# Performance work log

Hardware: AMD Instinct MI355X
Metric: run time of the kernel (lower is better)

## Reference

```python
import jax, jax.numpy as jnp
import numpy as np

N = 102400      # total agents across all groups
GROUP = 50      # agents per group
G = N // GROUP  # 2048 groups
E = 128         # embedding_dim
H = 512         # h_dim


def setup_inputs() -> dict:
    key = jax.random.key(0)
    k1, k2, k3, k4, k5, k6 = jax.random.split(key, 6)
    hist_enc = jax.random.normal(k1, (N, H), dtype=jnp.float32)
    hist_pos_batch = jax.random.normal(k2, (N, 2), dtype=jnp.float32)
    # group boundaries: 0, 50, 100, ..., N  (len = G+1)
    seq_start_end = (jnp.arange(G + 1, dtype=jnp.int32) * GROUP)
    # spatial_embedding: Linear(2, E)
    Ws = jax.random.normal(k3, (2, E), dtype=jnp.float32) * (1.0 / np.sqrt(2.0))
    bs = jax.random.normal(k4, (E,), dtype=jnp.float32) * 0.01
    # mlp_pre_pool: Linear(E + H, H)
    Wm = jax.random.normal(k5, (E + H, H), dtype=jnp.float32) * (1.0 / np.sqrt(E + H))
    bm = jax.random.normal(k6, (H,), dtype=jnp.float32) * 0.01
    return {
        "hist_enc": hist_enc,
        "hist_pos_batch": hist_pos_batch,
        "seq_start_end": seq_start_end,
        "Ws": Ws, "bs": bs, "Wm": Wm, "bm": bm,
    }


def reference(hist_enc, hist_pos_batch, seq_start_end, Ws, bs, Wm, bm):
    # The original torch loop builds all n^2 pairs per group but keeps only
    # curr_pool_h[0:1], i.e. row i=0 -> pooled vector for the group's FIRST agent.
    # rel[i=0, j] = pos[j] - pos[start]; hidden index is j; max over j.
    n = hist_enc.shape[0]
    num_groups = seq_start_end.shape[0] - 1
    # segment id of each agent: group g covers [sse[g], sse[g+1])
    seg_ids = jnp.searchsorted(seq_start_end, jnp.arange(n, dtype=seq_start_end.dtype), side="right") - 1
    starts = seq_start_end[:-1]                      # [G]
    anchor = hist_pos_batch[starts][seg_ids]         # [N,2] pos of group's first agent
    rel = hist_pos_batch - anchor                    # [N,2]
    emb = jax.nn.relu(rel @ Ws + bs)                 # [N,E]
    h_in = jnp.concatenate([hist_enc, emb], axis=1)  # [N,E+H]
    pooled = jax.nn.relu(h_in @ Wm + bm)             # [N,H]
    out = jax.ops.segment_max(pooled, seg_ids, num_segments=num_groups)  # [G,H]
    return out
```

## Files before the change

kernel.cpp:

```cpp
#include <hip/hip_runtime.h>


typedef __bf16 bf16x8 __attribute__((ext_vector_type(8)));
typedef float floatx4 __attribute__((ext_vector_type(4)));

constexpr int NR = 102400;
constexpr int NG = 2048;
constexpr int E  = 128;
constexpr int H  = 512;
constexpr int KD = 640;
constexpr int BM = 128, BN = 128, BK = 32;
constexpr int FM = 64, FN = 256;
constexpr int NKT = KD / BK;
constexpr int KH  = H / BK;

__device__ inline unsigned short f2bf(float f) {
    unsigned u = __float_as_uint(f);
    u += 0x7FFF + ((u >> 16) & 1u);
    return (unsigned short)(u >> 16);
}

__device__ inline unsigned pk2(float lo, float hi) {
    return __builtin_amdgcn_perm(__float_as_uint(hi) + 0x8000u,
                                 __float_as_uint(lo) + 0x8000u, 0x07060302u);
}

__device__ inline void async16(const void* g, void* l) {
    __builtin_amdgcn_global_load_lds(
        (const __attribute__((address_space(1))) unsigned int*)g,
        (__attribute__((address_space(3))) unsigned int*)l, 16, 0, 0);
}

__global__ __launch_bounds__(256) void prep3(
    const float* __restrict__ pos, const int* __restrict__ sse,
    const float* __restrict__ Wm, unsigned short* __restrict__ WmT,
    int* __restrict__ segArr, float* __restrict__ relA)
{
    const int b = blockIdx.x;
    const int t = threadIdx.x;
    __shared__ float tile[64][65];
    if (b < 400) {
        if (!segArr) return;
        const int i = b * 256 + t;
        int l = 0, r = NG + 1;
        while (l < r) { int m = (l + r) >> 1; if (sse[m] <= i) l = m + 1; else r = m; }
        const int g = l - 1;
        segArr[i] = g;
        const int a = sse[g];
        relA[2 * i + 0] = pos[2 * i + 0] - pos[2 * a + 0];
        relA[2 * i + 1] = pos[2 * i + 1] - pos[2 * a + 1];
    } else {
        const int bb = b - 400;
        const int kb = (bb % 10) * 64, nb = (bb / 10) * 64;
        const int tx = t & 63, tq = t >> 6;
#pragma unroll
        for (int i = 0; i < 16; ++i) {
            const int k = tq * 16 + i;
            tile[k][tx] = Wm[(size_t)(kb + k) * H + nb + tx];
        }
        __syncthreads();
#pragma unroll
        for (int i = 0; i < 16; ++i) {
            const int n = tq * 16 + i;
            WmT[(size_t)(nb + n) * KD + kb + tx] = f2bf(tile[tx][n]);
        }
    }
}

__global__ __launch_bounds__(256, 3) void pool_fused(
    const float* __restrict__ hist_enc,
    const int*   __restrict__ sse,
    const int*   __restrict__ segArr,
    const float* __restrict__ relA,
    const float* __restrict__ Ws,
    const float* __restrict__ bs,
    const unsigned short* __restrict__ WmT,
    const float* __restrict__ bm,
    float*       __restrict__ out)
{
    __shared__ __attribute__((aligned(16))) unsigned short As2[2][FM * BK];
    __shared__ __attribute__((aligned(16))) unsigned short Bs2[2][FN * BK];
    __shared__ float2 relRow[FM];
    __shared__ int segRow[FM];
    __shared__ int bnd[3];
    __shared__ int Pmax[4][FN + 4];

    const int t   = threadIdx.x;
    const int bid = blockIdx.x;
    const int rowTile = (bid >> 4) * 8 + (bid & 7);
    const int colTile = (bid >> 3) & 1;
    const int rowBase = rowTile * FM;
    const int cTile   = colTile * FN;

    const int lane  = t & 63;
    const int wv    = t >> 6;
    const int wc    = wv * 64;
    const int lcol  = lane & 15;
    const int lquad = lane >> 4;

    const int sR   = lane >> 2;
    const int phys = lane & 3;
    const unsigned short* gB[4];
#pragma unroll
    for (int s = 0; s < 4; ++s) {
        const int row = wv * 64 + s * 16 + sR;
        const int cl  = phys ^ ((row >> 1) & 3);
        gB[s] = WmT + (size_t)(cTile + row) * KD + cl * 8;
    }
    auto issueB = [&](int kt, int buf) {
        const int ko = kt * BK;
#pragma unroll
        for (int s = 0; s < 4; ++s)
            async16(gB[s] + ko, &Bs2[buf][wv * 2048 + s * 512]);
    };

    const int arow = t >> 2, ach = t & 3;
    const int aoff = arow * BK + (ach ^ ((arow >> 1) & 3)) * 8;
    const float* gA = hist_enc + (size_t)(rowBase + arow) * H + ach * 8;

    issueB(0, 0);

    if (t < FM) {
        segRow[t] = segArr[rowBase + t];
        relRow[t] = *(const float2*)&relA[2 * (rowBase + t)];
    }
    if (t >= FM && t < FM + 3) bnd[t - FM] = FM;
    for (int idx = t; idx < 4 * (FN + 4); idx += 256) ((int*)Pmax)[idx] = 0;

    {
        const float4 h0 = *(const float4*)(gA);
        const float4 h1 = *(const float4*)(gA + 4);
        uint4 u;
        u.x = pk2(h0.x, h0.y); u.y = pk2(h0.z, h0.w);
        u.z = pk2(h1.x, h1.y); u.w = pk2(h1.z, h1.w);
        *(uint4*)&As2[0][aoff] = u;
    }
    __syncthreads();
    if (t < FM - 1) {
        const int s0 = segRow[t], s1 = segRow[t + 1];
        if (s1 != s0) bnd[s1 - segRow[0] - 1] = t + 1;
    }

    floatx4 acc[4][4];
#pragma unroll
    for (int m = 0; m < 4; ++m)
#pragma unroll
        for (int n = 0; n < 4; ++n) acc[m][n] = (floatx4){0.f, 0.f, 0.f, 0.f};

    for (int kt = 0; kt < NKT; ++kt) {
        __syncthreads();
        const int nxt = kt + 1;
        float4 w0a, w0b, w1a, w1b, ba, bb;
        float r0 = 0.f, r1 = 0.f;
        bool hist = true;
        if (nxt < NKT) {
            issueB(nxt, nxt & 1);
            if (nxt < KH) {
                w0a = *(const float4*)(gA + nxt * BK);
                w0b = *(const float4*)(gA + nxt * BK + 4);
            } else {
                hist = false;
                const int e0 = nxt * BK - H + ach * 8;
                w0a = *(const float4*)&Ws[e0];     w0b = *(const float4*)&Ws[e0 + 4];
                w1a = *(const float4*)&Ws[E + e0]; w1b = *(const float4*)&Ws[E + e0 + 4];
                ba  = *(const float4*)&bs[e0];     bb  = *(const float4*)&bs[e0 + 4];
                const float2 rr = relRow[arow];
                r0 = rr.x; r1 = rr.y;
            }
        }

        const unsigned short* A = As2[kt & 1];
        const unsigned short* B = Bs2[kt & 1];
        bf16x8 af[4], bfr[4];
#pragma unroll
        for (int mt = 0; mt < 4; ++mt) {
            const int R  = mt * 16 + lcol;
            const int pc = lquad ^ ((R >> 1) & 3);
            af[mt] = *(const bf16x8*)&A[R * BK + pc * 8];
        }
#pragma unroll
        for (int nt = 0; nt < 4; ++nt) {
            const int R  = wc + nt * 16 + lcol;
            const int pc = lquad ^ ((R >> 1) & 3);
            bfr[nt] = *(const bf16x8*)&B[R * BK + pc * 8];
        }
#pragma unroll
        for (int mt = 0; mt < 4; ++mt)
#pragma unroll
            for (int nt = 0; nt < 4; ++nt)
                acc[mt][nt] = __builtin_amdgcn_mfma_f32_16x16x32_bf16(af[mt], bfr[nt], acc[mt][nt], 0, 0, 0);

        if (nxt < NKT) {
            uint4 u;
            if (hist) {
                u.x = pk2(w0a.x, w0a.y); u.y = pk2(w0a.z, w0a.w);
                u.z = pk2(w0b.x, w0b.y); u.w = pk2(w0b.z, w0b.w);
            } else {
                const float v0 = fmaxf(r0 * w0a.x + r1 * w1a.x + ba.x, 0.f);
                const float v1 = fmaxf(r0 * w0a.y + r1 * w1a.y + ba.y, 0.f);
                const float v2 = fmaxf(r0 * w0a.z + r1 * w1a.z + ba.z, 0.f);
                const float v3 = fmaxf(r0 * w0a.w + r1 * w1a.w + ba.w, 0.f);
                const float v4 = fmaxf(r0 * w0b.x + r1 * w1b.x + bb.x, 0.f);
                const float v5 = fmaxf(r0 * w0b.y + r1 * w1b.y + bb.y, 0.f);
                const float v6 = fmaxf(r0 * w0b.z + r1 * w1b.z + bb.z, 0.f);
                const float v7 = fmaxf(r0 * w0b.w + r1 * w1b.w + bb.w, 0.f);
                u.x = pk2(v0, v1); u.y = pk2(v2, v3);
                u.z = pk2(v4, v5); u.w = pk2(v6, v7);
            }
            *(uint4*)&As2[nxt & 1][aoff] = u;
        }
    }

    const int b0 = bnd[0], b1 = bnd[1], b2 = bnd[2];
    const int segBase = segRow[0];

#pragma unroll
    for (int nt = 0; nt < 4; ++nt) {
        const int col  = wc + nt * 16 + lcol;
        const float bias = bm[cTile + col];
        float pm[4] = {0.f, 0.f, 0.f, 0.f};
#pragma unroll
        for (int mt = 0; mt < 4; ++mt) {
#pragma unroll
            for (int r = 0; r < 4; ++r) {
                const int lr = mt * 16 + lquad * 4 + r;
                const int ls = (lr >= b0) + (lr >= b1) + (lr >= b2);
                const float v = fmaxf(acc[mt][nt][r] + bias, 0.f);
                pm[ls] = fmaxf(pm[ls], v);
            }
        }
#pragma unroll
        for (int ls = 0; ls < 4; ++ls)
            if (pm[ls] > 0.f)
                atomicMax(&Pmax[ls][col], __float_as_int(pm[ls]));
    }
    __syncthreads();

    for (int idx = t; idx < 4 * FN; idx += 256) {
        const int ls = idx >> 8, col = idx & (FN - 1);
        if (ls > 0 && bnd[ls - 1] >= FM) continue;
        const int seg = segBase + ls;
        const int v   = Pmax[ls][col];
        const int gs  = sse[seg], ge = sse[seg + 1];
        float* dst = &out[(size_t)seg * H + cTile + col];
        if (gs >= rowBase && ge <= rowBase + FM) {
            *dst = __int_as_float(v);
        } else {
            atomicMax((int*)dst, v);
        }
    }
}

constexpr int LDAF = 40;
__global__ __launch_bounds__(256) void pool_mfma_fb(
    const float* __restrict__ hist_enc, const float* __restrict__ pos,
    const int* __restrict__ sse, const float* __restrict__ Ws,
    const float* __restrict__ bs, const unsigned short* __restrict__ WmT,
    const float* __restrict__ bm, float* __restrict__ out)
{
    __shared__ __attribute__((aligned(16))) unsigned short As[BM][LDAF];
    __shared__ __attribute__((aligned(16))) unsigned short Bs[BN][LDAF];
    __shared__ float relRow[BM][2];
    __shared__ int   segRow[BM];
    __shared__ int   bnd[3];
    __shared__ int   Pmax[4][BN + 4];

    const int t = threadIdx.x;
    const int cTile = blockIdx.x * BN;
    const int rowBase = blockIdx.y * BM;

    if (t < BM) {
        const int i = rowBase + t;
        int l = 0, r = NG + 1;
        while (l < r) { int m = (l + r) >> 1; if (sse[m] <= i) l = m + 1; else r = m; }
        const int g = l - 1;
        segRow[t] = g;
        const int a = sse[g];
        relRow[t][0] = pos[2 * i + 0] - pos[2 * a + 0];
        relRow[t][1] = pos[2 * i + 1] - pos[2 * a + 1];
    }
    if (t >= BM && t < BM + 3) bnd[t - BM] = BM;
    for (int idx = t; idx < 4 * (BN + 4); idx += 256) ((int*)Pmax)[idx] = 0;
    __syncthreads();
    if (t < BM - 1) {
        const int s0 = segRow[t], s1 = segRow[t + 1];
        if (s1 != s0) bnd[s1 - segRow[0] - 1] = t + 1;
    }

    const int lane = t & 63, wv = t >> 6;
    const int wr = (wv >> 1) * 64, wc = (wv & 1) * 64;
    const int lcol = lane & 15, lquad = lane >> 4;

    floatx4 acc[4][4];
#pragma unroll
    for (int m = 0; m < 4; ++m)
#pragma unroll
        for (int n = 0; n < 4; ++n) acc[m][n] = (floatx4){0.f, 0.f, 0.f, 0.f};

    for (int kt = 0; kt < KD / BK; ++kt) {
        const int k0 = kt * BK;
        float4 av[4]; uint4 bv[2];
        if (k0 < H) {
#pragma unroll
            for (int i = 0; i < 4; ++i) {
                const int idx = i * 256 + t;
                const int row = idx >> 3, kq = (idx & 7) * 4;
                av[i] = *(const float4*)&hist_enc[(size_t)(rowBase + row) * H + k0 + kq];
            }
        } else {
#pragma unroll
            for (int i = 0; i < 4; ++i) {
                const int idx = i * 256 + t;
                const int row = idx >> 3, kq = (idx & 7) * 4;
                const int e = k0 - H + kq;
                const float4 w0 = *(const float4*)&Ws[e];
                const float4 w1 = *(const float4*)&Ws[E + e];
                const float4 b4 = *(const float4*)&bs[e];
                const float r0 = relRow[row][0], r1 = relRow[row][1];
                av[i].x = fmaxf(r0 * w0.x + r1 * w1.x + b4.x, 0.f);
                av[i].y = fmaxf(r0 * w0.y + r1 * w1.y + b4.y, 0.f);
                av[i].z = fmaxf(r0 * w0.z + r1 * w1.z + b4.z, 0.f);
                av[i].w = fmaxf(r0 * w0.w + r1 * w1.w + b4.w, 0.f);
            }
        }
#pragma unroll
        for (int i = 0; i < 2; ++i) {
            const int idx = i * 256 + t;
            const int n = idx >> 2, q = idx & 3;
            bv[i] = *(const uint4*)&WmT[(size_t)(cTile + n) * KD + k0 + q * 8];
        }
        __syncthreads();
#pragma unroll
        for (int i = 0; i < 4; ++i) {
            const int idx = i * 256 + t;
            const int row = idx >> 3, kq = (idx & 7) * 4;
            ushort4 p;
            p.x = f2bf(av[i].x); p.y = f2bf(av[i].y);
            p.z = f2bf(av[i].z); p.w = f2bf(av[i].w);
            *(ushort4*)&As[row][kq] = p;
        }
#pragma unroll
        for (int i = 0; i < 2; ++i) {
            const int idx = i * 256 + t;
            const int n = idx >> 2, q = idx & 3;
            *(uint4*)&Bs[n][q * 8] = bv[i];
        }
        __syncthreads();

        bf16x8 af[4], bfr[4];
#pragma unroll
        for (int mt = 0; mt < 4; ++mt)
            af[mt] = *(const bf16x8*)&As[wr + mt * 16 + lcol][lquad * 8];
#pragma unroll
        for (int nt = 0; nt < 4; ++nt)
            bfr[nt] = *(const bf16x8*)&Bs[wc + nt * 16 + lcol][lquad * 8];
#pragma unroll
        for (int mt = 0; mt < 4; ++mt)
#pragma unroll
            for (int nt = 0; nt < 4; ++nt)
                acc[mt][nt] = __builtin_amdgcn_mfma_f32_16x16x32_bf16(af[mt], bfr[nt], acc[mt][nt], 0, 0, 0);
    }

    const int b0 = bnd[0], b1 = bnd[1], b2 = bnd[2];
    const int segBase = segRow[0];
#pragma unroll
    for (int nt = 0; nt < 4; ++nt) {
        const int col = wc + nt * 16 + lcol;
        const float bias = bm[cTile + col];
        float pm[4] = {0.f, 0.f, 0.f, 0.f};
#pragma unroll
        for (int mt = 0; mt < 4; ++mt) {
#pragma unroll
            for (int r = 0; r < 4; ++r) {
                const int lr = wr + mt * 16 + lquad * 4 + r;
                const int ls = (lr >= b0) + (lr >= b1) + (lr >= b2);
                const float v = fmaxf(acc[mt][nt][r] + bias, 0.f);
                pm[ls] = fmaxf(pm[ls], v);
            }
        }
#pragma unroll
        for (int ls = 0; ls < 4; ++ls)
            if (pm[ls] > 0.f) atomicMax(&Pmax[ls][col], __float_as_int(pm[ls]));
    }
    __syncthreads();
    for (int idx = t; idx < 4 * BN; idx += 256) {
        const int ls = idx >> 7, col = idx & 127;
        if (ls > 0 && bnd[ls - 1] >= BM) continue;
        const int seg = segBase + ls;
        const int v = Pmax[ls][col];
        const int gs = sse[seg], ge = sse[seg + 1];
        float* dst = &out[(size_t)seg * H + cTile + col];
        if (gs >= rowBase && ge <= rowBase + BM) *dst = __int_as_float(v);
        else atomicMax((int*)dst, v);
    }
}

extern "C" void kernel_launch(void* const* d_in, const int* in_sizes, int n_in,
                              void* d_out, int out_size, void* d_ws, size_t ws_size,
                              hipStream_t stream) {
    const float* hist_enc = (const float*)d_in[0];
    const float* pos      = (const float*)d_in[1];
    const int*   sse      = (const int*)  d_in[2];
    const float* Ws       = (const float*)d_in[3];
    const float* bs       = (const float*)d_in[4];
    const float* Wm       = (const float*)d_in[5];
    const float* bm       = (const float*)d_in[6];
    float*       out      = (float*)d_out;

    const size_t needWmT = (size_t)H * KD * 2;
    const size_t needSeg = (size_t)NR * 4;
    const size_t needRel = (size_t)NR * 2 * 4;
    unsigned short* WmT  = (unsigned short*)d_ws;
    int*            segA = (int*)  ((char*)d_ws + needWmT);
    float*          relA = (float*)((char*)d_ws + needWmT + needSeg);

    hipMemsetAsync(out, 0, (size_t)out_size * sizeof(float), stream);

    if (ws_size >= needWmT + needSeg + needRel) {
        prep3<<<480, 256, 0, stream>>>(pos, sse, Wm, WmT, segA, relA);
        pool_fused<<<3200, 256, 0, stream>>>(hist_enc, sse, segA, relA, Ws, bs, WmT, bm, out);
    } else {
        prep3<<<480, 256, 0, stream>>>(pos, sse, Wm, WmT, nullptr, nullptr);
        pool_mfma_fb<<<dim3(H / BN, NR / BM), 256, 0, stream>>>(hist_enc, pos, sse, Ws, bs, WmT, bm, out);
    }
}
```

Measured before the change: 412.8 us.

## Switch fused pool kernel to 128x128 tiles with 2x2 waves and deeper A prefetch

Reshapes the fused GEMM+segment-max kernel from 64x256 block tiles, where each wave took a 64-column strip, to 128x128 tiles split over a 2x2 wave grid. hist_enc rows are now prefetched two K-steps ahead in registers, and the main loop is fully unrolled. Launch bounds rise to 4 blocks per CU. The aim is a more balanced A/B load per block and more latency hiding on the global fp32 loads, at the cost of more registers and up to 3 segment boundaries per 128-row tile.

```diff
diff --git a/kernel.cpp b/kernel.cpp
--- a/kernel.cpp
+++ b/kernel.cpp
@@ -10,7 +10,6 @@
 constexpr int H  = 512;
 constexpr int KD = 640;
 constexpr int BM = 128, BN = 128, BK = 32;
-constexpr int FM = 64, FN = 256;
 constexpr int NKT = KD / BK;
 constexpr int KH  = H / BK;
 
@@ -67,7 +66,7 @@
     }
 }
 
-__global__ __launch_bounds__(256, 3) void pool_fused(
+__global__ __launch_bounds__(256, 4) void pool_fused2(
     const float* __restrict__ hist_enc,
     const int*   __restrict__ sse,
     const int*   __restrict__ segArr,
@@ -78,65 +77,94 @@
     const float* __restrict__ bm,
     float*       __restrict__ out)
 {
-    __shared__ __attribute__((aligned(16))) unsigned short As2[2][FM * BK];
-    __shared__ __attribute__((aligned(16))) unsigned short Bs2[2][FN * BK];
-    __shared__ float2 relRow[FM];
-    __shared__ int segRow[FM];
+    __shared__ __attribute__((aligned(16))) unsigned short As2[2][BM * BK];
+    __shared__ __attribute__((aligned(16))) unsigned short Bs2[2][BN * BK];
+    __shared__ float2 relRow[BM];
+    __shared__ int segRow[BM];
     __shared__ int bnd[3];
-    __shared__ int Pmax[4][FN + 4];
+    __shared__ int Pmax[4][BN + 4];
 
     const int t   = threadIdx.x;
     const int bid = blockIdx.x;
-    const int rowTile = (bid >> 4) * 8 + (bid & 7);
-    const int colTile = (bid >> 3) & 1;
-    const int rowBase = rowTile * FM;
-    const int cTile   = colTile * FN;
+    const int rowTile = (bid >> 5) * 8 + (bid & 7);
+    const int colTile = (bid >> 3) & 3;
+    const int rowBase = rowTile * BM;
+    const int cTile   = colTile * BN;
 
     const int lane  = t & 63;
     const int wv    = t >> 6;
-    const int wc    = wv * 64;
+    const int wr    = (wv >> 1) * 64;
+    const int wc    = (wv & 1) * 64;
     const int lcol  = lane & 15;
     const int lquad = lane >> 4;
 
-    const int sR   = lane >> 2;
-    const int phys = lane & 3;
-    const unsigned short* gB[4];
-#pragma unroll
-    for (int s = 0; s < 4; ++s) {
-        const int row = wv * 64 + s * 16 + sR;
-        const int cl  = phys ^ ((row >> 1) & 3);
-        gB[s] = WmT + (size_t)(cTile + row) * KD + cl * 8;
-    }
+    const int sRow0 = wv * 32 + (lane >> 2);
+    const int sRow1 = sRow0 + 16;
+    const int phys  = lane & 3;
+    const int cl0   = phys ^ ((sRow0 >> 1) & 3);
+    const int cl1   = phys ^ ((sRow1 >> 1) & 3);
+    const unsigned short* gB0 = WmT + (size_t)(cTile + sRow0) * KD + cl0 * 8;
+    const unsigned short* gB1 = WmT + (size_t)(cTile + sRow1) * KD + cl1 * 8;
     auto issueB = [&](int kt, int buf) {
         const int ko = kt * BK;
-#pragma unroll
-        for (int s = 0; s < 4; ++s)
-            async16(gB[s] + ko, &Bs2[buf][wv * 2048 + s * 512]);
+        async16(gB0 + ko, &Bs2[buf][wv * 1024]);
+        async16(gB1 + ko, &Bs2[buf][wv * 1024 + 512]);
     };
 
-    const int arow = t >> 2, ach = t & 3;
-    const int aoff = arow * BK + (ach ^ ((arow >> 1) & 3)) * 8;
-    const float* gA = hist_enc + (size_t)(rowBase + arow) * H + ach * 8;
+    const int arow = t >> 1;
+    const int half = t & 1;
+    const int sw   = (arow >> 1) & 3;
+    const float* gA = hist_enc + (size_t)(rowBase + arow) * H + half * 16;
+
+    auto loadA = [&](int T, float4* f) {
+        f[0] = *(const float4*)(gA + T * BK);
+        f[1] = *(const float4*)(gA + T * BK + 4);
+        f[2] = *(const float4*)(gA + T * BK + 8);
+        f[3] = *(const float4*)(gA + T * BK + 12);
+    };
+    auto writeA = [&](int buf, const float4* f) {
+        uint4 u0, u1;
+        u0.x = pk2(f[0].x, f[0].y); u0.y = pk2(f[0].z, f[0].w);
+        u0.z = pk2(f[1].x, f[1].y); u0.w = pk2(f[1].z, f[1].w);
+        u1.x = pk2(f[2].x, f[2].y); u1.y = pk2(f[2].z, f[2].w);
+        u1.z = pk2(f[3].x, f[3].y); u1.w = pk2(f[3].z, f[3].w);
+        const int c0 = half * 2;
+        *(uint4*)&As2[buf][arow * BK + ((c0    ) ^ sw) * 8] = u0;
+        *(uint4*)&As2[buf][arow * BK + ((c0 + 1) ^ sw) * 8] = u1;
+    };
+    auto embA = [&](int T, int buf) {
+        const int e0 = T * BK - H + half * 16;
+        const float2 rr = relRow[arow];
+        float4 f[4];
+#pragma unroll
+        for (int q = 0; q < 4; ++q) {
+            const float4 w0 = *(const float4*)&Ws[e0 + q * 4];
+            const float4 w1 = *(const float4*)&Ws[E + e0 + q * 4];
+            const float4 b4 = *(const float4*)&bs[e0 + q * 4];
+            f[q].x = fmaxf(rr.x * w0.x + rr.y * w1.x + b4.x, 0.f);
+            f[q].y = fmaxf(rr.x * w0.y + rr.y * w1.y + b4.y, 0.f);
+            f[q].z = fmaxf(rr.x * w0.z + rr.y * w1.z + b4.z, 0.f);
+            f[q].w = fmaxf(rr.x * w0.w + rr.y * w1.w + b4.w, 0.f);
+        }
+        writeA(buf, f);
+    };
 
     issueB(0, 0);
 
-    if (t < FM) {
+    if (t < BM) {
         segRow[t] = segArr[rowBase + t];
         relRow[t] = *(const float2*)&relA[2 * (rowBase + t)];
     }
-    if (t >= FM && t < FM + 3) bnd[t - FM] = FM;
-    for (int idx = t; idx < 4 * (FN + 4); idx += 256) ((int*)Pmax)[idx] = 0;
-
-    {
-        const float4 h0 = *(const float4*)(gA);
-        const float4 h1 = *(const float4*)(gA + 4);
-        uint4 u;
-        u.x = pk2(h0.x, h0.y); u.y = pk2(h0.z, h0.w);
-        u.z = pk2(h1.x, h1.y); u.w = pk2(h1.z, h1.w);
-        *(uint4*)&As2[0][aoff] = u;
-    }
+    if (t >= BM && t < BM + 3) bnd[t - BM] = BM;
+    for (int idx = t; idx < 4 * (BN + 4); idx += 256) ((int*)Pmax)[idx] = 0;
+
+    float4 rA[2][4];
+    loadA(0, rA[0]);
+    writeA(0, rA[0]);
+    loadA(1, rA[1]);
+
     __syncthreads();
-    if (t < FM - 1) {
+    if (t < BM - 1) {
         const int s0 = segRow[t], s1 = segRow[t + 1];
         if (s1 != s0) bnd[s1 - segRow[0] - 1] = t + 1;
     }
@@ -147,34 +175,18 @@
 #pragma unroll
         for (int n = 0; n < 4; ++n) acc[m][n] = (floatx4){0.f, 0.f, 0.f, 0.f};
 
+#pragma unroll
     for (int kt = 0; kt < NKT; ++kt) {
         __syncthreads();
-        const int nxt = kt + 1;
-        float4 w0a, w0b, w1a, w1b, ba, bb;
-        float r0 = 0.f, r1 = 0.f;
-        bool hist = true;
-        if (nxt < NKT) {
-            issueB(nxt, nxt & 1);
-            if (nxt < KH) {
-                w0a = *(const float4*)(gA + nxt * BK);
-                w0b = *(const float4*)(gA + nxt * BK + 4);
-            } else {
-                hist = false;
-                const int e0 = nxt * BK - H + ach * 8;
-                w0a = *(const float4*)&Ws[e0];     w0b = *(const float4*)&Ws[e0 + 4];
-                w1a = *(const float4*)&Ws[E + e0]; w1b = *(const float4*)&Ws[E + e0 + 4];
-                ba  = *(const float4*)&bs[e0];     bb  = *(const float4*)&bs[e0 + 4];
-                const float2 rr = relRow[arow];
-                r0 = rr.x; r1 = rr.y;
-            }
-        }
+        if (kt + 1 < NKT) issueB(kt + 1, (kt + 1) & 1);
+        if (kt + 2 < KH)  loadA(kt + 2, rA[kt & 1]);
 
         const unsigned short* A = As2[kt & 1];
         const unsigned short* B = Bs2[kt & 1];
         bf16x8 af[4], bfr[4];
 #pragma unroll
         for (int mt = 0; mt < 4; ++mt) {
-            const int R  = mt * 16 + lcol;
+            const int R  = wr + mt * 16 + lcol;
             const int pc = lquad ^ ((R >> 1) & 3);
             af[mt] = *(const bf16x8*)&A[R * BK + pc * 8];
         }
@@ -190,24 +202,9 @@
             for (int nt = 0; nt < 4; ++nt)
                 acc[mt][nt] = __builtin_amdgcn_mfma_f32_16x16x32_bf16(af[mt], bfr[nt], acc[mt][nt], 0, 0, 0);
 
-        if (nxt < NKT) {
-            uint4 u;
-            if (hist) {
-                u.x = pk2(w0a.x, w0a.y); u.y = pk2(w0a.z, w0a.w);
-                u.z = pk2(w0b.x, w0b.y); u.w = pk2(w0b.z, w0b.w);
-            } else {
-                const float v0 = fmaxf(r0 * w0a.x + r1 * w1a.x + ba.x, 0.f);
-                const float v1 = fmaxf(r0 * w0a.y + r1 * w1a.y + ba.y, 0.f);
-                const float v2 = fmaxf(r0 * w0a.z + r1 * w1a.z + ba.z, 0.f);
-                const float v3 = fmaxf(r0 * w0a.w + r1 * w1a.w + ba.w, 0.f);
-                const float v4 = fmaxf(r0 * w0b.x + r1 * w1b.x + bb.x, 0.f);
-                const float v5 = fmaxf(r0 * w0b.y + r1 * w1b.y + bb.y, 0.f);
-                const float v6 = fmaxf(r0 * w0b.z + r1 * w1b.z + bb.z, 0.f);
-                const float v7 = fmaxf(r0 * w0b.w + r1 * w1b.w + bb.w, 0.f);
-                u.x = pk2(v0, v1); u.y = pk2(v2, v3);
-                u.z = pk2(v4, v5); u.w = pk2(v6, v7);
-            }
-            *(uint4*)&As2[nxt & 1][aoff] = u;
+        if (kt + 1 < NKT) {
+            if (kt + 1 < KH) writeA((kt + 1) & 1, rA[(kt + 1) & 1]);
+            else             embA(kt + 1, (kt + 1) & 1);
         }
     }
 
@@ -223,7 +220,7 @@
         for (int mt = 0; mt < 4; ++mt) {
 #pragma unroll
             for (int r = 0; r < 4; ++r) {
-                const int lr = mt * 16 + lquad * 4 + r;
+                const int lr = wr + mt * 16 + lquad * 4 + r;
                 const int ls = (lr >= b0) + (lr >= b1) + (lr >= b2);
                 const float v = fmaxf(acc[mt][nt][r] + bias, 0.f);
                 pm[ls] = fmaxf(pm[ls], v);
@@ -236,14 +233,14 @@
     }
     __syncthreads();
 
-    for (int idx = t; idx < 4 * FN; idx += 256) {
-        const int ls = idx >> 8, col = idx & (FN - 1);
-        if (ls > 0 && bnd[ls - 1] >= FM) continue;
+    for (int idx = t; idx < 4 * BN; idx += 256) {
+        const int ls = idx >> 7, col = idx & 127;
+        if (ls > 0 && bnd[ls - 1] >= BM) continue;
         const int seg = segBase + ls;
         const int v   = Pmax[ls][col];
         const int gs  = sse[seg], ge = sse[seg + 1];
         float* dst = &out[(size_t)seg * H + cTile + col];
-        if (gs >= rowBase && ge <= rowBase + FM) {
+        if (gs >= rowBase && ge <= rowBase + BM) {
             *dst = __int_as_float(v);
         } else {
             atomicMax((int*)dst, v);
@@ -418,7 +415,7 @@
 
     if (ws_size >= needWmT + needSeg + needRel) {
         prep3<<<480, 256, 0, stream>>>(pos, sse, Wm, WmT, segA, relA);
-        pool_fused<<<3200, 256, 0, stream>>>(hist_enc, sse, segA, relA, Ws, bs, WmT, bm, out);
+        pool_fused2<<<3200, 256, 0, stream>>>(hist_enc, sse, segA, relA, Ws, bs, WmT, bm, out);
     } else {
         prep3<<<480, 256, 0, stream>>>(pos, sse, Wm, WmT, nullptr, nullptr);
         pool_mfma_fb<<<dim3(H / BN, NR / BM), 256, 0, stream>>>(hist_enc, pos, sse, Ws, bs, WmT, bm, out);
```

After: 411.7 us. About the same (-0.3%).

## Stream A rows directly into registers and keep full B slab in LDS

Applied to the files above, without the earlier changes.

Replaces the double-buffered LDS GEMM with a kernel where each block loads the full 64-column by 640-K slice of the transposed weight into LDS once. Each wave streams its own 64 rows of hist_enc straight from global memory into registers with a two-stage prefetch, packing to bf16 in registers, so A never goes through LDS and the K loop has no barriers. The segment-max epilogue now uses per-lane masks and cross-lane shuffles with direct atomicMax to the output, replacing the shared-memory Pmax pass. In exchange, each hist_enc row is reread by eight column blocks instead of two, LDS use rises to 80KB so occupancy drops to two blocks per CU, and the register-resident A tiles have uncoalesced strided global loads.

```diff
diff --git a/kernel.cpp b/kernel.cpp
--- a/kernel.cpp
+++ b/kernel.cpp
@@ -10,7 +10,6 @@
 constexpr int H  = 512;
 constexpr int KD = 640;
 constexpr int BM = 128, BN = 128, BK = 32;
-constexpr int FM = 64, FN = 256;
 constexpr int NKT = KD / BK;
 constexpr int KH  = H / BK;
 
@@ -25,10 +24,11 @@
                                  __float_as_uint(lo) + 0x8000u, 0x07060302u);
 }
 
-__device__ inline void async16(const void* g, void* l) {
-    __builtin_amdgcn_global_load_lds(
-        (const __attribute__((address_space(1))) unsigned int*)g,
-        (__attribute__((address_space(3))) unsigned int*)l, 16, 0, 0);
+__device__ inline bf16x8 pk8(float4 a, float4 b) {
+    union { uint4 u; bf16x8 v; } c;
+    c.u.x = pk2(a.x, a.y); c.u.y = pk2(a.z, a.w);
+    c.u.z = pk2(b.x, b.y); c.u.w = pk2(b.z, b.w);
+    return c.v;
 }
 
 __global__ __launch_bounds__(256) void prep3(
@@ -67,7 +67,7 @@
     }
 }
 
-__global__ __launch_bounds__(256, 3) void pool_fused(
+__global__ __launch_bounds__(256, 2) void pool_stream(
     const float* __restrict__ hist_enc,
     const int*   __restrict__ sse,
     const int*   __restrict__ segArr,
@@ -78,68 +78,64 @@
     const float* __restrict__ bm,
     float*       __restrict__ out)
 {
-    __shared__ __attribute__((aligned(16))) unsigned short As2[2][FM * BK];
-    __shared__ __attribute__((aligned(16))) unsigned short Bs2[2][FN * BK];
-    __shared__ float2 relRow[FM];
-    __shared__ int segRow[FM];
-    __shared__ int bnd[3];
-    __shared__ int Pmax[4][FN + 4];
+    __shared__ __attribute__((aligned(16))) unsigned short Bs[NKT * 64 * 32];
 
     const int t   = threadIdx.x;
     const int bid = blockIdx.x;
-    const int rowTile = (bid >> 4) * 8 + (bid & 7);
-    const int colTile = (bid >> 3) & 1;
-    const int rowBase = rowTile * FM;
-    const int cTile   = colTile * FN;
+    const int x     = bid & 7;
+    const int q     = bid >> 3;
+    const int col   = q & 7;
+    const int chunk = (q >> 3) * 8 + x;
+    const int rowBase = chunk * 256;
+    const int cTile   = col * 64;
 
     const int lane  = t & 63;
     const int wv    = t >> 6;
-    const int wc    = wv * 64;
     const int lcol  = lane & 15;
     const int lquad = lane >> 4;
 
-    const int sR   = lane >> 2;
-    const int phys = lane & 3;
-    const unsigned short* gB[4];
-#pragma unroll
-    for (int s = 0; s < 4; ++s) {
-        const int row = wv * 64 + s * 16 + sR;
-        const int cl  = phys ^ ((row >> 1) & 3);
-        gB[s] = WmT + (size_t)(cTile + row) * KD + cl * 8;
-    }
-    auto issueB = [&](int kt, int buf) {
-        const int ko = kt * BK;
-#pragma unroll
-        for (int s = 0; s < 4; ++s)
-            async16(gB[s] + ko, &Bs2[buf][wv * 2048 + s * 512]);
-    };
-
-    const int arow = t >> 2, ach = t & 3;
-    const int aoff = arow * BK + (ach ^ ((arow >> 1) & 3)) * 8;
-    const float* gA = hist_enc + (size_t)(rowBase + arow) * H + ach * 8;
-
-    issueB(0, 0);
-
-    if (t < FM) {
-        segRow[t] = segArr[rowBase + t];
-        relRow[t] = *(const float2*)&relA[2 * (rowBase + t)];
-    }
-    if (t >= FM && t < FM + 3) bnd[t - FM] = FM;
-    for (int idx = t; idx < 4 * (FN + 4); idx += 256) ((int*)Pmax)[idx] = 0;
-
     {
-        const float4 h0 = *(const float4*)(gA);
-        const float4 h1 = *(const float4*)(gA + 4);
-        uint4 u;
-        u.x = pk2(h0.x, h0.y); u.y = pk2(h0.z, h0.w);
-        u.z = pk2(h1.x, h1.y); u.w = pk2(h1.z, h1.w);
-        *(uint4*)&As2[0][aoff] = u;
-    }
+        const unsigned short* src = WmT + (size_t)cTile * KD;
+#pragma unroll
+        for (int i = 0; i < 20; ++i) {
+            const int idx = i * 256 + t;
+            const int r = idx / 80, c8 = idx % 80;
+            const uint4 v = *(const uint4*)&src[(size_t)r * KD + c8 * 8];
+            const int kt = c8 >> 2;
+            const int j  = (c8 & 3) ^ ((r >> 1) & 3);
+            *(uint4*)&Bs[kt * 2048 + r * 32 + j * 8] = v;
+        }
+    }
+
+    const int wbase = rowBase + wv * 64;
+    const float* pA[4];
+#pragma unroll
+    for (int mt = 0; mt < 4; ++mt)
+        pA[mt] = hist_enc + (size_t)(wbase + mt * 16 + lcol) * H + lquad * 8;
+
+    float2 relm[4];
+#pragma unroll
+    for (int mt = 0; mt < 4; ++mt)
+        relm[mt] = *(const float2*)&relA[2 * (wbase + mt * 16 + lcol)];
+
+    float bias[4];
+#pragma unroll
+    for (int nt = 0; nt < 4; ++nt) bias[nt] = bm[cTile + nt * 16 + lcol];
+
+    const int s0 = segArr[wbase];
+    const int bA = sse[s0 + 1];
+    const int bB = (s0 + 2 <= NG) ? sse[s0 + 2] : 0x7fffffff;
+
+    float4 st[2][4][2];
+#pragma unroll
+    for (int mt = 0; mt < 4; ++mt) {
+        st[0][mt][0] = *(const float4*)(pA[mt] + 0);
+        st[0][mt][1] = *(const float4*)(pA[mt] + 4);
+        st[1][mt][0] = *(const float4*)(pA[mt] + BK);
+        st[1][mt][1] = *(const float4*)(pA[mt] + BK + 4);
+    }
+
     __syncthreads();
-    if (t < FM - 1) {
-        const int s0 = segRow[t], s1 = segRow[t + 1];
-        if (s1 != s0) bnd[s1 - segRow[0] - 1] = t + 1;
-    }
 
     floatx4 acc[4][4];
 #pragma unroll
@@ -147,106 +143,91 @@
 #pragma unroll
         for (int n = 0; n < 4; ++n) acc[m][n] = (floatx4){0.f, 0.f, 0.f, 0.f};
 
+#pragma unroll
     for (int kt = 0; kt < NKT; ++kt) {
-        __syncthreads();
-        const int nxt = kt + 1;
-        float4 w0a, w0b, w1a, w1b, ba, bb;
-        float r0 = 0.f, r1 = 0.f;
-        bool hist = true;
-        if (nxt < NKT) {
-            issueB(nxt, nxt & 1);
-            if (nxt < KH) {
-                w0a = *(const float4*)(gA + nxt * BK);
-                w0b = *(const float4*)(gA + nxt * BK + 4);
-            } else {
-                hist = false;
-                const int e0 = nxt * BK - H + ach * 8;
-                w0a = *(const float4*)&Ws[e0];     w0b = *(const float4*)&Ws[e0 + 4];
-                w1a = *(const float4*)&Ws[E + e0]; w1b = *(const float4*)&Ws[E + e0 + 4];
-                ba  = *(const float4*)&bs[e0];     bb  = *(const float4*)&bs[e0 + 4];
-                const float2 rr = relRow[arow];
-                r0 = rr.x; r1 = rr.y;
-            }
-        }
-
-        const unsigned short* A = As2[kt & 1];
-        const unsigned short* B = Bs2[kt & 1];
-        bf16x8 af[4], bfr[4];
-#pragma unroll
-        for (int mt = 0; mt < 4; ++mt) {
-            const int R  = mt * 16 + lcol;
-            const int pc = lquad ^ ((R >> 1) & 3);
-            af[mt] = *(const bf16x8*)&A[R * BK + pc * 8];
-        }
+        bf16x8 af[4];
+        if (kt < KH) {
+#pragma unroll
+            for (int mt = 0; mt < 4; ++mt)
+                af[mt] = pk8(st[kt & 1][mt][0], st[kt & 1][mt][1]);
+            if (kt + 2 < KH) {
+#pragma unroll
+                for (int mt = 0; mt < 4; ++mt) {
+                    st[kt & 1][mt][0] = *(const float4*)(pA[mt] + (kt + 2) * BK);
+                    st[kt & 1][mt][1] = *(const float4*)(pA[mt] + (kt + 2) * BK + 4);
+                }
+            }
+        } else {
+            const int e0 = (kt - KH) * BK + lquad * 8;
+            const float4 w0a = *(const float4*)&Ws[e0];
+            const float4 w0b = *(const float4*)&Ws[e0 + 4];
+            const float4 w1a = *(const float4*)&Ws[E + e0];
+            const float4 w1b = *(const float4*)&Ws[E + e0 + 4];
+            const float4 ba4 = *(const float4*)&bs[e0];
+            const float4 bb4 = *(const float4*)&bs[e0 + 4];
+#pragma unroll
+            for (int mt = 0; mt < 4; ++mt) {
+                const float r0 = relm[mt].x, r1 = relm[mt].y;
+                float4 fa, fb;
+                fa.x = fmaxf(r0 * w0a.x + r1 * w1a.x + ba4.x, 0.f);
+                fa.y = fmaxf(r0 * w0a.y + r1 * w1a.y + ba4.y, 0.f);
+                fa.z = fmaxf(r0 * w0a.z + r1 * w1a.z + ba4.z, 0.f);
+                fa.w = fmaxf(r0 * w0a.w + r1 * w1a.w + ba4.w, 0.f);
+                fb.x = fmaxf(r0 * w0b.x + r1 * w1b.x + bb4.x, 0.f);
+                fb.y = fmaxf(r0 * w0b.y + r1 * w1b.y + bb4.y, 0.f);
+                fb.z = fmaxf(r0 * w0b.z + r1 * w1b.z + bb4.z, 0.f);
+                fb.w = fmaxf(r0 * w0b.w + r1 * w1b.w + bb4.w, 0.f);
+                af[mt] = pk8(fa, fb);
+            }
+        }
+
+        bf16x8 bfr[4];
 #pragma unroll
         for (int nt = 0; nt < 4; ++nt) {
-            const int R  = wc + nt * 16 + lcol;
-            const int pc = lquad ^ ((R >> 1) & 3);
-            bfr[nt] = *(const bf16x8*)&B[R * BK + pc * 8];
-        }
+            const int c  = nt * 16 + lcol;
+            const int pc = lquad ^ ((c >> 1) & 3);
+            bfr[nt] = *(const bf16x8*)&Bs[kt * 2048 + c * 32 + pc * 8];
+        }
+
+        __builtin_amdgcn_s_setprio(1);
 #pragma unroll
         for (int mt = 0; mt < 4; ++mt)
 #pragma unroll
             for (int nt = 0; nt < 4; ++nt)
                 acc[mt][nt] = __builtin_amdgcn_mfma_f32_16x16x32_bf16(af[mt], bfr[nt], acc[mt][nt], 0, 0, 0);
-
-        if (nxt < NKT) {
-            uint4 u;
-            if (hist) {
-                u.x = pk2(w0a.x, w0a.y); u.y = pk2(w0a.z, w0a.w);
-                u.z = pk2(w0b.x, w0b.y); u.w = pk2(w0b.z, w0b.w);
-            } else {
-                const float v0 = fmaxf(r0 * w0a.x + r1 * w1a.x + ba.x, 0.f);
-                const float v1 = fmaxf(r0 * w0a.y + r1 * w1a.y + ba.y, 0.f);
-                const float v2 = fmaxf(r0 * w0a.z + r1 * w1a.z + ba.z, 0.f);
-                const float v3 = fmaxf(r0 * w0a.w + r1 * w1a.w + ba.w, 0.f);
-                const float v4 = fmaxf(r0 * w0b.x + r1 * w1b.x + bb.x, 0.f);
-                const float v5 = fmaxf(r0 * w0b.y + r1 * w1b.y + bb.y, 0.f);
-                const float v6 = fmaxf(r0 * w0b.z + r1 * w1b.z + bb.z, 0.f);
-                const float v7 = fmaxf(r0 * w0b.w + r1 * w1b.w + bb.w, 0.f);
-                u.x = pk2(v0, v1); u.y = pk2(v2, v3);
-                u.z = pk2(v4, v5); u.w = pk2(v6, v7);
-            }
-            *(uint4*)&As2[nxt & 1][aoff] = u;
-        }
-    }
-
-    const int b0 = bnd[0], b1 = bnd[1], b2 = bnd[2];
-    const int segBase = segRow[0];
-
+        __builtin_amdgcn_s_setprio(0);
+    }
+
+    float pm0[4] = {0.f, 0.f, 0.f, 0.f};
+    float pm1[4] = {0.f, 0.f, 0.f, 0.f};
+    float pm2[4] = {0.f, 0.f, 0.f, 0.f};
 #pragma unroll
     for (int nt = 0; nt < 4; ++nt) {
-        const int col  = wc + nt * 16 + lcol;
-        const float bias = bm[cTile + col];
-        float pm[4] = {0.f, 0.f, 0.f, 0.f};
 #pragma unroll
         for (int mt = 0; mt < 4; ++mt) {
 #pragma unroll
-            for (int r = 0; r < 4; ++r) {
-                const int lr = mt * 16 + lquad * 4 + r;
-                const int ls = (lr >= b0) + (lr >= b1) + (lr >= b2);
-                const float v = fmaxf(acc[mt][nt][r] + bias, 0.f);
-                pm[ls] = fmaxf(pm[ls], v);
-            }
-        }
-#pragma unroll
-        for (int ls = 0; ls < 4; ++ls)
-            if (pm[ls] > 0.f)
-                atomicMax(&Pmax[ls][col], __float_as_int(pm[ls]));
-    }
-    __syncthreads();
-
-    for (int idx = t; idx < 4 * FN; idx += 256) {
-        const int ls = idx >> 8, col = idx & (FN - 1);
-        if (ls > 0 && bnd[ls - 1] >= FM) continue;
-        const int seg = segBase + ls;
-        const int v   = Pmax[ls][col];
-        const int gs  = sse[seg], ge = sse[seg + 1];
-        float* dst = &out[(size_t)seg * H + cTile + col];
-        if (gs >= rowBase && ge <= rowBase + FM) {
-            *dst = __int_as_float(v);
-        } else {
-            atomicMax((int*)dst, v);
+            for (int rr = 0; rr < 4; ++rr) {
+                const int rowAbs = wbase + mt * 16 + lquad * 4 + rr;
+                const float v = fmaxf(acc[mt][nt][rr] + bias[nt], 0.f);
+                const bool geA = rowAbs >= bA;
+                const bool geB = rowAbs >= bB;
+                pm0[nt] = fmaxf(pm0[nt], (!geA)         ? v : 0.f);
+                pm1[nt] = fmaxf(pm1[nt], (geA && !geB)  ? v : 0.f);
+                pm2[nt] = fmaxf(pm2[nt], (geB)          ? v : 0.f);
+            }
+        }
+    }
+#pragma unroll
+    for (int s = 0; s < 3; ++s) {
+#pragma unroll
+        for (int nt = 0; nt < 4; ++nt) {
+            float v = (s == 0) ? pm0[nt] : (s == 1) ? pm1[nt] : pm2[nt];
+            v = fmaxf(v, __shfl_xor(v, 16));
+            v = fmaxf(v, __shfl_xor(v, 32));
+            if (lquad == 0 && v > 0.f) {
+                float* dst = &out[(size_t)(s0 + s) * H + cTile + nt * 16 + lcol];
+                atomicMax((int*)dst, __float_as_int(v));
+            }
         }
     }
 }
@@ -259,7 +240,7 @@
     const float* __restrict__ bm, float* __restrict__ out)
 {
     __shared__ __attribute__((aligned(16))) unsigned short As[BM][LDAF];
-    __shared__ __attribute__((aligned(16))) unsigned short Bs[BN][LDAF];
+    __shared__ __attribute__((aligned(16))) unsigned short Bsb[BN][LDAF];
     __shared__ float relRow[BM][2];
     __shared__ int   segRow[BM];
     __shared__ int   bnd[3];
@@ -343,7 +324,7 @@
         for (int i = 0; i < 2; ++i) {
             const int idx = i * 256 + t;
             const int n = idx >> 2, q = idx & 3;
-            *(uint4*)&Bs[n][q * 8] = bv[i];
+            *(uint4*)&Bsb[n][q * 8] = bv[i];
         }
         __syncthreads();
 
@@ -353,7 +334,7 @@
             af[mt] = *(const bf16x8*)&As[wr + mt * 16 + lcol][lquad * 8];
 #pragma unroll
         for (int nt = 0; nt < 4; ++nt)
-            bfr[nt] = *(const bf16x8*)&Bs[wc + nt * 16 + lcol][lquad * 8];
+            bfr[nt] = *(const bf16x8*)&Bsb[wc + nt * 16 + lcol][lquad * 8];
 #pragma unroll
         for (int mt = 0; mt < 4; ++mt)
 #pragma unroll
@@ -418,7 +399,7 @@
 
     if (ws_size >= needWmT + needSeg + needRel) {
         prep3<<<480, 256, 0, stream>>>(pos, sse, Wm, WmT, segA, relA);
-        pool_fused<<<3200, 256, 0, stream>>>(hist_enc, sse, segA, relA, Ws, bs, WmT, bm, out);
+        pool_stream<<<3200, 256, 0, stream>>>(hist_enc, sse, segA, relA, Ws, bs, WmT, bm, out);
     } else {
         prep3<<<480, 256, 0, stream>>>(pos, sse, Wm, WmT, nullptr, nullptr);
         pool_mfma_fb<<<dim3(H / BN, NR / BM), 256, 0, stream>>>(hist_enc, pos, sse, Ws, bs, WmT, bm, out);
```

Measured after the change: 444.2 us. 7.6% more time.
